# Optimization experiments

Measured on AMD Instinct MI355X. Metric: run time of the kernel, lower is better.

The kernel has to match this reference:

```python
import jax, jax.numpy as jnp
import numpy as np
from jax import lax

EPS = 1e-6
MATCH_THRESHOLD = 0.3
N_DISCRETE_STEPS = 5
DT = 0.01
TWO_PI = 2.0 * np.pi


def setup_inputs() -> dict:
    key = jax.random.key(0)
    ks = jax.random.split(key, 6)
    N, M, D, H, n_osc = 8192, 8192, 4, 64, 28
    detections_t = jax.random.normal(ks[0], (N, D), dtype=jnp.float32)
    detections_t1 = jax.random.normal(ks[1], (M, D), dtype=jnp.float32)
    phase_W1 = jax.random.normal(ks[2], (D, H), dtype=jnp.float32) * (1.0 / np.sqrt(D))
    phase_b1 = jax.random.normal(ks[3], (H,), dtype=jnp.float32) * 0.05
    phase_W2 = jax.random.normal(ks[4], (H, n_osc), dtype=jnp.float32) * (1.0 / np.sqrt(H))
    phase_b2 = jax.random.normal(ks[5], (n_osc,), dtype=jnp.float32) * 0.05
    # fixed oscillator frequencies buffer: [2]*4 + [6]*8 + [40]*16
    frequencies = jnp.concatenate([
        jnp.full((4,), 2.0, jnp.float32),
        jnp.full((8,), 6.0, jnp.float32),
        jnp.full((16,), 40.0, jnp.float32),
    ])
    return {
        'detections_t': detections_t,
        'detections_t1': detections_t1,
        'phase_W1': phase_W1,
        'phase_b1': phase_b1,
        'phase_W2': phase_W2,
        'phase_b2': phase_b2,
        'frequencies': frequencies,
    }


def _encode_phase(x, W1, b1, W2, b2):
    h = jax.nn.relu(x @ W1 + b1)
    raw = h @ W2 + b2
    return raw % TWO_PI  # [N, n_osc]


def _similarity(phase_a, phase_b):
    # real(sum_k e^{i a_k} e^{-i b_k}) = cos(a)@cos(b).T + sin(a)@sin(b).T
    ca, sa = jnp.cos(phase_a), jnp.sin(phase_a)
    cb, sb = jnp.cos(phase_b), jnp.sin(phase_b)
    na = jnp.sqrt(jnp.sum(ca * ca + sa * sa, axis=-1, keepdims=True)) + EPS  # [N,1]
    nb = jnp.sqrt(jnp.sum(cb * cb + sb * sb, axis=-1, keepdims=True)) + EPS  # [M,1]
    sim = (ca @ cb.T + sa @ sb.T) / (na * nb.T)  # [N, M]
    return sim


def reference(detections_t, detections_t1, phase_W1, phase_b1, phase_W2, phase_b2, frequencies):
    phase_t = _encode_phase(detections_t, phase_W1, phase_b1, phase_W2, phase_b2)
    phase_t1 = _encode_phase(detections_t1, phase_W1, phase_b1, phase_W2, phase_b2)

    # uncoupled phase advance (n_discrete_steps fixed small loop)
    phase = phase_t
    for _ in range(N_DISCRETE_STEPS):
        phase = (phase + TWO_PI * frequencies * DT) % TWO_PI

    sim = _similarity(phase, phase_t1)  # [N, M]

    N = detections_t.shape[0]
    M = detections_t1.shape[0]
    max_sims = jnp.max(sim, axis=1)
    max_idxs = jnp.argmax(sim, axis=1)
    order = jnp.argsort(-max_sims)  # descending

    def body(i, carry):
        matches, used = carry
        idx = order[i]
        j = max_idxs[idx]
        ok = jnp.logical_and(jnp.logical_not(used[j]), max_sims[idx] > MATCH_THRESHOLD)
        matches = matches.at[idx].set(jnp.where(ok, j, -1))
        used = used.at[j].set(jnp.logical_or(used[j], ok))
        return (matches, used)

    matches0 = jnp.full((N,), -1, dtype=jnp.int32)
    used0 = jnp.zeros((M,), dtype=bool)
    matches, _ = lax.fori_loop(0, N, body, (matches0, used0))
    return (matches, sim)
```

## Files before the change

kernel.cpp:

```cpp
#include <hip/hip_runtime.h>
#include <math.h>

#define NR 8192
#define N_OSC 28
#define TWO_PI_F 6.28318530717958647692f
#define PLANE 524288

typedef __attribute__((ext_vector_type(8))) short s16x8;
typedef __attribute__((ext_vector_type(16))) float f32x16;
typedef __attribute__((ext_vector_type(4))) float f32x4;
typedef __attribute__((ext_vector_type(4))) unsigned int u32x4;

#define AS3(p) ((__attribute__((address_space(3))) void*)(p))
#define AS1C(p) ((const __attribute__((address_space(1))) void*)(p))

__device__ __forceinline__ float modpos(float x) {
    float r = fmodf(x, TWO_PI_F);
    if (r < 0.0f) r += TWO_PI_F;
    return r;
}
__device__ __forceinline__ unsigned fmono(float f) {
    unsigned u = __float_as_uint(f);
    return (u & 0x80000000u) ? ~u : (u | 0x80000000u);
}
__device__ __forceinline__ unsigned short f2bf(float f) {
    unsigned u = __float_as_uint(f);
    return (unsigned short)((u + 0x7FFFu + ((u >> 16) & 1u)) >> 16);
}
__device__ __forceinline__ float bf2f(unsigned short h) {
    return __uint_as_float(((unsigned)h) << 16);
}


__global__ __launch_bounds__(256, 1) void encode_kernel(
    const float* __restrict__ detA, const float* __restrict__ detB,
    const float* __restrict__ W1, const float* __restrict__ b1,
    const float* __restrict__ W2, const float* __restrict__ b2,
    const float* __restrict__ freq,
    unsigned short* __restrict__ tabA, unsigned short* __restrict__ tabB,
    float* __restrict__ normA, float* __restrict__ normB)
{
    __shared__ float sW1[4 * 64];
    __shared__ float sb1[64];
    __shared__ float sW2[64 * N_OSC];
    __shared__ float sb2[N_OSC];
    __shared__ float sDelta[N_OSC];

    int t = threadIdx.x;
    for (int i = t; i < 4 * 64; i += 256) sW1[i] = W1[i];
    for (int i = t; i < 64; i += 256) sb1[i] = b1[i];
    for (int i = t; i < 64 * N_OSC; i += 256) sW2[i] = W2[i];
    for (int i = t; i < N_OSC; i += 256) {
        sb2[i] = b2[i];
        sDelta[i] = (TWO_PI_F * freq[i]) * 0.01f;
    }
    __syncthreads();

    int gid = blockIdx.x * 256 + t;
    bool isA = gid < NR;
    int row = isA ? gid : gid - NR;
    const float* det = isA ? detA : detB;
    unsigned short* tab = isA ? tabA : tabB;
    float* nrm = isA ? normA : normB;

    float4 xv = *(const float4*)(det + (size_t)row * 4);
    float x0 = xv.x, x1 = xv.y, x2 = xv.z, x3 = xv.w;

    float h[64];
#pragma unroll
    for (int j = 0; j < 64; ++j) {
        float a = x0 * sW1[0 * 64 + j];
        a += x1 * sW1[1 * 64 + j];
        a += x2 * sW1[2 * 64 + j];
        a += x3 * sW1[3 * 64 + j];
        a += sb1[j];
        h[j] = fmaxf(a, 0.0f);
    }

    float raw[N_OSC];
#pragma unroll
    for (int o = 0; o < N_OSC; ++o) raw[o] = 0.0f;
#pragma unroll
    for (int j = 0; j < 64; ++j) {
        float hj = h[j];
#pragma unroll
        for (int o = 0; o < N_OSC; ++o) raw[o] += hj * sW2[j * N_OSC + o];
    }

    unsigned h2[32], m2[32], l2[32];
#pragma unroll
    for (int i = 0; i < 32; ++i) { h2[i] = 0u; m2[i] = 0u; l2[i] = 0u; }

    float csum = 0.0f;
#pragma unroll
    for (int o = 0; o < N_OSC; ++o) {
        float p = raw[o] + sb2[o];
        p = modpos(p);
        if (isA) {
            float d = sDelta[o];
#pragma unroll
            for (int s = 0; s < 5; ++s) { p = modpos(p + d); }
        }
        float sn, cs;
        sincosf(p, &sn, &cs);
        csum += cs * cs + sn * sn;
        {
            unsigned short v0 = f2bf(cs); float r1 = cs - bf2f(v0);
            unsigned short v1 = f2bf(r1); float r2 = r1 - bf2f(v1);
            unsigned short v2 = f2bf(r2);
            const int k = o, i = k >> 1, sh = (k & 1) * 16;
            h2[i] |= ((unsigned)v0) << sh;
            m2[i] |= ((unsigned)v1) << sh;
            l2[i] |= ((unsigned)v2) << sh;
        }
        {
            unsigned short v0 = f2bf(sn); float r1 = sn - bf2f(v0);
            unsigned short v1 = f2bf(r1); float r2 = r1 - bf2f(v1);
            unsigned short v2 = f2bf(r2);
            const int k = 28 + o, i = k >> 1, sh = (k & 1) * 16;
            h2[i] |= ((unsigned)v0) << sh;
            m2[i] |= ((unsigned)v1) << sh;
            l2[i] |= ((unsigned)v2) << sh;
        }
    }

    size_t gbase = (size_t)(row >> 5) * 2048 + (size_t)(row & 31) * 8;
#pragma unroll
    for (int c = 0; c < 8; ++c) {
        size_t off = gbase + (size_t)(c >> 1) * 512 + (size_t)(c & 1) * 256;
        u32x4 vh, vm, vl;
#pragma unroll
        for (int e = 0; e < 4; ++e) {
            vh[e] = h2[c * 4 + e]; vm[e] = m2[c * 4 + e]; vl[e] = l2[c * 4 + e];
        }
        *(u32x4*)(tab + off) = vh;
        *(u32x4*)(tab + PLANE + off) = vm;
        *(u32x4*)(tab + 2 * PLANE + off) = vl;
    }
    nrm[row] = 1.0f / (sqrtf(csum) + 1e-6f);
}

#define MFMA(a, b, c) __builtin_amdgcn_mfma_f32_32x32x16_bf16((a), (b), (c), 0, 0, 0)

__global__ __launch_bounds__(256, 1) void sim_kernel(
    const unsigned short* __restrict__ tabA, const unsigned short* __restrict__ tabB,
    const float* __restrict__ normA, const float* __restrict__ normB,
    float* __restrict__ simOut, unsigned long long* __restrict__ rowMax)
{
    __shared__ __align__(16) unsigned char smem[69632];
    unsigned short* Ash = (unsigned short*)smem;

    int bid = blockIdx.x;
    int swz = (bid & 7) * 512 + (bid >> 3);
    int bx = swz & 63, by = swz >> 6;
    int r0 = by * 128, c0 = bx * 128;

    int t = threadIdx.x, w = t >> 6, l = t & 63;
    int wr = w >> 1, wc = w & 1;
    int lrow = l & 31;
    int gB = (c0 + wc * 64) >> 5;
    int gr0 = r0 >> 5;
    size_t l8 = (size_t)l * 8;

#define GLD(tab, pl, g, ks) \
    (*(const s16x8*)((tab) + (size_t)(pl) * PLANE + (size_t)(g) * 2048 + (size_t)(ks) * 512 + l8))

    s16x8 bh0[4], bh1[4], bm0[4], bm1[4], bl0[4], bl1[4];
#pragma unroll
    for (int ks = 0; ks < 4; ++ks) {
        bh0[ks] = GLD(tabB, 0, gB, ks);  bh1[ks] = GLD(tabB, 0, gB + 1, ks);
        bm0[ks] = GLD(tabB, 1, gB, ks);  bm1[ks] = GLD(tabB, 1, gB + 1, ks);
        bl0[ks] = GLD(tabB, 2, gB, ks);  bl1[ks] = GLD(tabB, 2, gB + 1, ks);
    }
#undef GLD

#pragma unroll
    for (int i = 0; i < 12; ++i) {
        int unit = w * 12 + i;
        int p = unit >> 4, rem = unit & 15;
        int g = rem >> 2, ks = rem & 3;
        const unsigned short* src = tabA + (size_t)p * PLANE
            + (size_t)(gr0 + g) * 2048 + (size_t)ks * 512 + l8;
        __builtin_amdgcn_global_load_lds(AS1C(src), AS3(Ash + unit * 512), 16, 0, 0);
    }
    __builtin_amdgcn_sched_barrier(0);
    __syncthreads();

    f32x16 acc00, acc01, acc10, acc11;
#pragma unroll
    for (int r = 0; r < 16; ++r) { acc00[r] = 0.f; acc01[r] = 0.f; acc10[r] = 0.f; acc11[r] = 0.f; }

    const char* Ab = (const char*)Ash + (size_t)wr * 8192 + (size_t)l * 16;
#define LDA(p, gg, ks) (*(const s16x8*)(Ab + ((p) * 16384 + (gg) * 4096 + (ks) * 1024)))

#pragma unroll
    for (int ks = 0; ks < 4; ++ks) {
        s16x8 ah0 = LDA(0, 0, ks), ah1 = LDA(0, 1, ks);
        s16x8 am0 = LDA(1, 0, ks), am1 = LDA(1, 1, ks);
        s16x8 al0 = LDA(2, 0, ks), al1 = LDA(2, 1, ks);

        acc00 = MFMA(ah0, bh0[ks], acc00); acc01 = MFMA(ah0, bh1[ks], acc01);
        acc10 = MFMA(ah1, bh0[ks], acc10); acc11 = MFMA(ah1, bh1[ks], acc11);
        acc00 = MFMA(ah0, bm0[ks], acc00); acc01 = MFMA(ah0, bm1[ks], acc01);
        acc10 = MFMA(ah1, bm0[ks], acc10); acc11 = MFMA(ah1, bm1[ks], acc11);
        acc00 = MFMA(am0, bh0[ks], acc00); acc01 = MFMA(am0, bh1[ks], acc01);
        acc10 = MFMA(am1, bh0[ks], acc10); acc11 = MFMA(am1, bh1[ks], acc11);
        acc00 = MFMA(am0, bm0[ks], acc00); acc01 = MFMA(am0, bm1[ks], acc01);
        acc10 = MFMA(am1, bm0[ks], acc10); acc11 = MFMA(am1, bm1[ks], acc11);
        acc00 = MFMA(ah0, bl0[ks], acc00); acc01 = MFMA(ah0, bl1[ks], acc01);
        acc10 = MFMA(ah1, bl0[ks], acc10); acc11 = MFMA(ah1, bl1[ks], acc11);
        acc00 = MFMA(al0, bh0[ks], acc00); acc01 = MFMA(al0, bh1[ks], acc01);
        acc10 = MFMA(al1, bh0[ks], acc10); acc11 = MFMA(al1, bh1[ks], acc11);
    }
#undef LDA

    float icn0 = normB[c0 + wc * 64 + lrow];
    float icn1 = normB[c0 + wc * 64 + 32 + lrow];

    __syncthreads();
    float* scr = (float*)(smem + w * 17408);

#pragma unroll
    for (int r = 0; r < 16; ++r) {
        int rd0 = (r & 3) + 8 * (r >> 2) + 4 * (l >> 5);
        float irn0 = normA[r0 + wr * 64 + rd0];
        scr[rd0 * 68 + lrow]      = acc00[r] * (irn0 * icn0);
        scr[rd0 * 68 + 32 + lrow] = acc01[r] * (irn0 * icn1);
        int rd1 = rd0 + 32;
        float irn1 = normA[r0 + wr * 64 + rd1];
        scr[rd1 * 68 + lrow]      = acc10[r] * (irn1 * icn0);
        scr[rd1 * 68 + 32 + lrow] = acc11[r] * (irn1 * icn1);
    }

#pragma unroll
    for (int s = 0; s < 16; ++s) {
        int lr = 4 * s + (l >> 4);
        f32x4 v = *(const f32x4*)&scr[lr * 68 + (l & 15) * 4];
        int grow = r0 + wr * 64 + lr;
        __builtin_nontemporal_store(v,
            (f32x4*)&simOut[(size_t)grow * NR + c0 + wc * 64 + (l & 15) * 4]);
    }

    {
        const float* rp = &scr[l * 68];
        float mv = -2.0f; int mc = 0;
#pragma unroll
        for (int c4 = 0; c4 < 16; ++c4) {
            f32x4 v = *(const f32x4*)&rp[c4 * 4];
#pragma unroll
            for (int e = 0; e < 4; ++e) {
                bool g = v[e] > mv;
                mv = g ? v[e] : mv;
                mc = g ? c4 * 4 + e : mc;
            }
        }
        int grow = r0 + wr * 64 + l;
        unsigned gcol = (unsigned)(c0 + wc * 64 + mc);
        unsigned long long key = ((unsigned long long)fmono(mv) << 32)
                               | (unsigned long long)(0xFFFFFFFFu - gcol);
        atomicMax(&rowMax[grow], key);
    }
}

__global__ __launch_bounds__(256) void rowwin_kernel(
    const unsigned long long* __restrict__ rowMax,
    unsigned long long* __restrict__ colWin,
    float* __restrict__ outMatches)
{
    int r = blockIdx.x * 256 + threadIdx.x;
    if (r >= NR) return;
    outMatches[r] = -1.0f;
    unsigned long long key = rowMax[r];
    unsigned m = (unsigned)(key >> 32);
    unsigned bits = (m & 0x80000000u) ? (m ^ 0x80000000u) : ~m;
    float ms = __uint_as_float(bits);
    unsigned col = 0xFFFFFFFFu - (unsigned)key;
    if (ms > 0.3f) {
        unsigned long long ck = ((unsigned long long)m << 32)
                              | (unsigned long long)(0xFFFFFFFFu - (unsigned)r);
        atomicMax(&colWin[col], ck);
    }
}

__global__ __launch_bounds__(256) void colfin_kernel(
    const unsigned long long* __restrict__ colWin,
    float* __restrict__ outMatches)
{
    int j = blockIdx.x * 256 + threadIdx.x;
    if (j >= NR) return;
    unsigned long long w = colWin[j];
    if (w != 0ull) {
        unsigned r = 0xFFFFFFFFu - (unsigned)w;
        outMatches[r] = (float)j;
    }
}

extern "C" void kernel_launch(void* const* d_in, const int* in_sizes, int n_in,
                              void* d_out, int out_size, void* d_ws, size_t ws_size,
                              hipStream_t stream) {
    const float* detA = (const float*)d_in[0];
    const float* detB = (const float*)d_in[1];
    const float* W1   = (const float*)d_in[2];
    const float* b1   = (const float*)d_in[3];
    const float* W2   = (const float*)d_in[4];
    const float* b2   = (const float*)d_in[5];
    const float* freq = (const float*)d_in[6];
    float* out = (float*)d_out;

    char* ws = (char*)d_ws;
    unsigned short* tabA = (unsigned short*)(ws);
    unsigned short* tabB = (unsigned short*)(ws + 3145728);
    float* normA = (float*)(ws + 6291456);
    float* normB = (float*)(ws + 6324224);
    unsigned long long* rowMax = (unsigned long long*)(ws + 6356992);
    unsigned long long* colWin = (unsigned long long*)(ws + 6422528);

    (void)hipMemsetAsync(rowMax, 0, NR * 8, stream);
    (void)hipMemsetAsync(colWin, 0, NR * 8, stream);

    encode_kernel<<<64, 256, 0, stream>>>(detA, detB, W1, b1, W2, b2, freq,
                                          tabA, tabB, normA, normB);
    sim_kernel<<<4096, 256, 0, stream>>>(tabA, tabB, normA, normB, out + NR, rowMax);
    rowwin_kernel<<<NR / 256, 256, 0, stream>>>(rowMax, colWin, out);
    colfin_kernel<<<NR / 256, 256, 0, stream>>>(colWin, out);
}
```

Before: 149.4 us.

## Fold norms into encoded phases, shrink sim tiles, compute row max from registers

Normalization is folded into the encode step by scaling cos and sin by the inverse norm before bf16 splitting, which drops the norm loads and multiplies from the similarity epilogue. The sim kernel moves to 64x128 tiles with 2 waves per block and twice as many blocks, and swaps the MFMA operand order so each lane's accumulators hold a row. The row argmax is then computed directly from accumulator registers plus a cross-half shuffle, instead of rescanning shared memory. The cost is a transposed shared-memory write pattern with stride 65 and more blocks each reloading the B tiles, plus slightly different rounding because normalization now happens before the bf16 split.

```diff
diff --git a/kernel.cpp b/kernel.cpp
--- a/kernel.cpp
+++ b/kernel.cpp
@@ -37,8 +37,7 @@
     const float* __restrict__ W1, const float* __restrict__ b1,
     const float* __restrict__ W2, const float* __restrict__ b2,
     const float* __restrict__ freq,
-    unsigned short* __restrict__ tabA, unsigned short* __restrict__ tabB,
-    float* __restrict__ normA, float* __restrict__ normB)
+    unsigned short* __restrict__ tabA, unsigned short* __restrict__ tabB)
 {
     __shared__ float sW1[4 * 64];
     __shared__ float sb1[64];
@@ -61,7 +60,6 @@
     int row = isA ? gid : gid - NR;
     const float* det = isA ? detA : detB;
     unsigned short* tab = isA ? tabA : tabB;
-    float* nrm = isA ? normA : normB;
 
     float4 xv = *(const float4*)(det + (size_t)row * 4);
     float x0 = xv.x, x1 = xv.y, x2 = xv.z, x3 = xv.w;
@@ -87,10 +85,7 @@
         for (int o = 0; o < N_OSC; ++o) raw[o] += hj * sW2[j * N_OSC + o];
     }
 
-    unsigned h2[32], m2[32], l2[32];
-#pragma unroll
-    for (int i = 0; i < 32; ++i) { h2[i] = 0u; m2[i] = 0u; l2[i] = 0u; }
-
+    float cv[N_OSC], sv[N_OSC];
     float csum = 0.0f;
 #pragma unroll
     for (int o = 0; o < N_OSC; ++o) {
@@ -103,9 +98,20 @@
         }
         float sn, cs;
         sincosf(p, &sn, &cs);
+        cv[o] = cs; sv[o] = sn;
         csum += cs * cs + sn * sn;
+    }
+    float irn = 1.0f / (sqrtf(csum) + 1e-6f);
+
+    unsigned h2[32], m2[32], l2[32];
+#pragma unroll
+    for (int i = 0; i < 32; ++i) { h2[i] = 0u; m2[i] = 0u; l2[i] = 0u; }
+
+#pragma unroll
+    for (int o = 0; o < N_OSC; ++o) {
         {
-            unsigned short v0 = f2bf(cs); float r1 = cs - bf2f(v0);
+            float x = cv[o] * irn;
+            unsigned short v0 = f2bf(x); float r1 = x - bf2f(v0);
             unsigned short v1 = f2bf(r1); float r2 = r1 - bf2f(v1);
             unsigned short v2 = f2bf(r2);
             const int k = o, i = k >> 1, sh = (k & 1) * 16;
@@ -114,7 +120,8 @@
             l2[i] |= ((unsigned)v2) << sh;
         }
         {
-            unsigned short v0 = f2bf(sn); float r1 = sn - bf2f(v0);
+            float x = sv[o] * irn;
+            unsigned short v0 = f2bf(x); float r1 = x - bf2f(v0);
             unsigned short v1 = f2bf(r1); float r2 = r1 - bf2f(v1);
             unsigned short v2 = f2bf(r2);
             const int k = 28 + o, i = k >> 1, sh = (k & 1) * 16;
@@ -137,27 +144,25 @@
         *(u32x4*)(tab + PLANE + off) = vm;
         *(u32x4*)(tab + 2 * PLANE + off) = vl;
     }
-    nrm[row] = 1.0f / (sqrtf(csum) + 1e-6f);
 }
 
 #define MFMA(a, b, c) __builtin_amdgcn_mfma_f32_32x32x16_bf16((a), (b), (c), 0, 0, 0)
 
-__global__ __launch_bounds__(256, 1) void sim_kernel(
+__global__ __launch_bounds__(128, 1) void sim_kernel(
     const unsigned short* __restrict__ tabA, const unsigned short* __restrict__ tabB,
-    const float* __restrict__ normA, const float* __restrict__ normB,
     float* __restrict__ simOut, unsigned long long* __restrict__ rowMax)
 {
-    __shared__ __align__(16) unsigned char smem[69632];
+    __shared__ __align__(16) unsigned char smem[33280];
     unsigned short* Ash = (unsigned short*)smem;
 
     int bid = blockIdx.x;
-    int swz = (bid & 7) * 512 + (bid >> 3);
+    int swz = (bid & 7) * 1024 + (bid >> 3);
     int bx = swz & 63, by = swz >> 6;
-    int r0 = by * 128, c0 = bx * 128;
+    int r0 = by * 64, c0 = bx * 128;
 
     int t = threadIdx.x, w = t >> 6, l = t & 63;
-    int wr = w >> 1, wc = w & 1;
-    int lrow = l & 31;
+    int wc = w;
+    int l31 = l & 31, h5 = l >> 5;
     int gB = (c0 + wc * 64) >> 5;
     int gr0 = r0 >> 5;
     size_t l8 = (size_t)l * 8;
@@ -177,7 +182,7 @@
 #pragma unroll
     for (int i = 0; i < 12; ++i) {
         int unit = w * 12 + i;
-        int p = unit >> 4, rem = unit & 15;
+        int p = unit >> 3, rem = unit & 7;
         int g = rem >> 2, ks = rem & 3;
         const unsigned short* src = tabA + (size_t)p * PLANE
             + (size_t)(gr0 + g) * 2048 + (size_t)ks * 512 + l8;
@@ -190,8 +195,8 @@
 #pragma unroll
     for (int r = 0; r < 16; ++r) { acc00[r] = 0.f; acc01[r] = 0.f; acc10[r] = 0.f; acc11[r] = 0.f; }
 
-    const char* Ab = (const char*)Ash + (size_t)wr * 8192 + (size_t)l * 16;
-#define LDA(p, gg, ks) (*(const s16x8*)(Ab + ((p) * 16384 + (gg) * 4096 + (ks) * 1024)))
+    const char* Ab = (const char*)Ash + (size_t)l * 16;
+#define LDA(p, g, ks) (*(const s16x8*)(Ab + (((p) * 8 + (g) * 4 + (ks)) * 1024)))
 
 #pragma unroll
     for (int ks = 0; ks < 4; ++ks) {
@@ -199,66 +204,71 @@
         s16x8 am0 = LDA(1, 0, ks), am1 = LDA(1, 1, ks);
         s16x8 al0 = LDA(2, 0, ks), al1 = LDA(2, 1, ks);
 
-        acc00 = MFMA(ah0, bh0[ks], acc00); acc01 = MFMA(ah0, bh1[ks], acc01);
-        acc10 = MFMA(ah1, bh0[ks], acc10); acc11 = MFMA(ah1, bh1[ks], acc11);
-        acc00 = MFMA(ah0, bm0[ks], acc00); acc01 = MFMA(ah0, bm1[ks], acc01);
-        acc10 = MFMA(ah1, bm0[ks], acc10); acc11 = MFMA(ah1, bm1[ks], acc11);
-        acc00 = MFMA(am0, bh0[ks], acc00); acc01 = MFMA(am0, bh1[ks], acc01);
-        acc10 = MFMA(am1, bh0[ks], acc10); acc11 = MFMA(am1, bh1[ks], acc11);
-        acc00 = MFMA(am0, bm0[ks], acc00); acc01 = MFMA(am0, bm1[ks], acc01);
-        acc10 = MFMA(am1, bm0[ks], acc10); acc11 = MFMA(am1, bm1[ks], acc11);
-        acc00 = MFMA(ah0, bl0[ks], acc00); acc01 = MFMA(ah0, bl1[ks], acc01);
-        acc10 = MFMA(ah1, bl0[ks], acc10); acc11 = MFMA(ah1, bl1[ks], acc11);
-        acc00 = MFMA(al0, bh0[ks], acc00); acc01 = MFMA(al0, bh1[ks], acc01);
-        acc10 = MFMA(al1, bh0[ks], acc10); acc11 = MFMA(al1, bh1[ks], acc11);
+        acc00 = MFMA(bh0[ks], ah0, acc00); acc01 = MFMA(bh1[ks], ah0, acc01);
+        acc10 = MFMA(bh0[ks], ah1, acc10); acc11 = MFMA(bh1[ks], ah1, acc11);
+        acc00 = MFMA(bm0[ks], ah0, acc00); acc01 = MFMA(bm1[ks], ah0, acc01);
+        acc10 = MFMA(bm0[ks], ah1, acc10); acc11 = MFMA(bm1[ks], ah1, acc11);
+        acc00 = MFMA(bh0[ks], am0, acc00); acc01 = MFMA(bh1[ks], am0, acc01);
+        acc10 = MFMA(bh0[ks], am1, acc10); acc11 = MFMA(bh1[ks], am1, acc11);
+        acc00 = MFMA(bm0[ks], am0, acc00); acc01 = MFMA(bm1[ks], am0, acc01);
+        acc10 = MFMA(bm0[ks], am1, acc10); acc11 = MFMA(bm1[ks], am1, acc11);
+        acc00 = MFMA(bl0[ks], ah0, acc00); acc01 = MFMA(bl1[ks], ah0, acc01);
+        acc10 = MFMA(bl0[ks], ah1, acc10); acc11 = MFMA(bl1[ks], ah1, acc11);
+        acc00 = MFMA(bh0[ks], al0, acc00); acc01 = MFMA(bh1[ks], al0, acc01);
+        acc10 = MFMA(bh0[ks], al1, acc10); acc11 = MFMA(bh1[ks], al1, acc11);
     }
 #undef LDA
 
-    float icn0 = normB[c0 + wc * 64 + lrow];
-    float icn1 = normB[c0 + wc * 64 + 32 + lrow];
+    int cbase = c0 + wc * 64 + 4 * h5;
+    unsigned long long key0 = 0ull, key1 = 0ull;
+#pragma unroll
+    for (int r = 0; r < 16; ++r) {
+        int pa = (r & 3) + 8 * (r >> 2);
+        unsigned col0 = (unsigned)(cbase + pa);
+        unsigned col1 = (unsigned)(cbase + 32 + pa);
+        unsigned long long k;
+        k = ((unsigned long long)fmono(acc00[r]) << 32) | (unsigned long long)(0xFFFFFFFFu - col0);
+        if (k > key0) key0 = k;
+        k = ((unsigned long long)fmono(acc01[r]) << 32) | (unsigned long long)(0xFFFFFFFFu - col1);
+        if (k > key0) key0 = k;
+        k = ((unsigned long long)fmono(acc10[r]) << 32) | (unsigned long long)(0xFFFFFFFFu - col0);
+        if (k > key1) key1 = k;
+        k = ((unsigned long long)fmono(acc11[r]) << 32) | (unsigned long long)(0xFFFFFFFFu - col1);
+        if (k > key1) key1 = k;
+    }
+    {
+        unsigned lo = (unsigned)key0, hi = (unsigned)(key0 >> 32);
+        unsigned olo = __shfl_xor(lo, 32, 64), ohi = __shfl_xor(hi, 32, 64);
+        unsigned long long o = ((unsigned long long)ohi << 32) | olo;
+        if (o > key0) key0 = o;
+        lo = (unsigned)key1; hi = (unsigned)(key1 >> 32);
+        olo = __shfl_xor(lo, 32, 64); ohi = __shfl_xor(hi, 32, 64);
+        o = ((unsigned long long)ohi << 32) | olo;
+        if (o > key1) key1 = o;
+    }
+    if (l < 32) {
+        atomicMax(&rowMax[r0 + l], key0);
+        atomicMax(&rowMax[r0 + 32 + l], key1);
+    }
 
     __syncthreads();
-    float* scr = (float*)(smem + w * 17408);
+    float* scr = (float*)(smem + w * 16640);
 
 #pragma unroll
     for (int r = 0; r < 16; ++r) {
-        int rd0 = (r & 3) + 8 * (r >> 2) + 4 * (l >> 5);
-        float irn0 = normA[r0 + wr * 64 + rd0];
-        scr[rd0 * 68 + lrow]      = acc00[r] * (irn0 * icn0);
-        scr[rd0 * 68 + 32 + lrow] = acc01[r] * (irn0 * icn1);
-        int rd1 = rd0 + 32;
-        float irn1 = normA[r0 + wr * 64 + rd1];
-        scr[rd1 * 68 + lrow]      = acc10[r] * (irn1 * icn0);
-        scr[rd1 * 68 + 32 + lrow] = acc11[r] * (irn1 * icn1);
+        int pa = (r & 3) + 8 * (r >> 2) + 4 * h5;
+        scr[l31 * 65 + pa]             = acc00[r];
+        scr[l31 * 65 + 32 + pa]        = acc01[r];
+        scr[(32 + l31) * 65 + pa]      = acc10[r];
+        scr[(32 + l31) * 65 + 32 + pa] = acc11[r];
     }
 
 #pragma unroll
     for (int s = 0; s < 16; ++s) {
         int lr = 4 * s + (l >> 4);
-        f32x4 v = *(const f32x4*)&scr[lr * 68 + (l & 15) * 4];
-        int grow = r0 + wr * 64 + lr;
+        f32x4 v = *(const f32x4*)&scr[lr * 65 + (l & 15) * 4];
         __builtin_nontemporal_store(v,
-            (f32x4*)&simOut[(size_t)grow * NR + c0 + wc * 64 + (l & 15) * 4]);
-    }
-
-    {
-        const float* rp = &scr[l * 68];
-        float mv = -2.0f; int mc = 0;
-#pragma unroll
-        for (int c4 = 0; c4 < 16; ++c4) {
-            f32x4 v = *(const f32x4*)&rp[c4 * 4];
-#pragma unroll
-            for (int e = 0; e < 4; ++e) {
-                bool g = v[e] > mv;
-                mv = g ? v[e] : mv;
-                mc = g ? c4 * 4 + e : mc;
-            }
-        }
-        int grow = r0 + wr * 64 + l;
-        unsigned gcol = (unsigned)(c0 + wc * 64 + mc);
-        unsigned long long key = ((unsigned long long)fmono(mv) << 32)
-                               | (unsigned long long)(0xFFFFFFFFu - gcol);
-        atomicMax(&rowMax[grow], key);
+            (f32x4*)&simOut[(size_t)(r0 + lr) * NR + c0 + wc * 64 + (l & 15) * 4]);
     }
 }
 
@@ -310,17 +320,15 @@
     char* ws = (char*)d_ws;
     unsigned short* tabA = (unsigned short*)(ws);
     unsigned short* tabB = (unsigned short*)(ws + 3145728);
-    float* normA = (float*)(ws + 6291456);
-    float* normB = (float*)(ws + 6324224);
-    unsigned long long* rowMax = (unsigned long long*)(ws + 6356992);
-    unsigned long long* colWin = (unsigned long long*)(ws + 6422528);
+    unsigned long long* rowMax = (unsigned long long*)(ws + 6291456);
+    unsigned long long* colWin = (unsigned long long*)(ws + 6356992);
 
     (void)hipMemsetAsync(rowMax, 0, NR * 8, stream);
     (void)hipMemsetAsync(colWin, 0, NR * 8, stream);
 
     encode_kernel<<<64, 256, 0, stream>>>(detA, detB, W1, b1, W2, b2, freq,
-                                          tabA, tabB, normA, normB);
-    sim_kernel<<<4096, 256, 0, stream>>>(tabA, tabB, normA, normB, out + NR, rowMax);
+                                          tabA, tabB);
+    sim_kernel<<<8192, 128, 0, stream>>>(tabA, tabB, out + NR, rowMax);
     rowwin_kernel<<<NR / 256, 256, 0, stream>>>(rowMax, colWin, out);
     colfin_kernel<<<NR / 256, 256, 0, stream>>>(colWin, out);
 }
```

Result: faster. 142.1 us (-4.9%).

## Stage B tile in LDS and stream A planes with double-buffered loads

Applied to the files above, without the earlier changes.

Moves the three B bf16 planes into shared memory instead of registers and streams A planes one at a time through two LDS buffers, overlapping the next plane's load with MFMA work on the current one. It relaxes launch bounds to permit higher occupancy and zeroes the rowMax/colWin buffers inside the encode kernel instead of separate memset calls. This trades register pressure for more LDS reads and extra barriers per tile.

```diff
diff --git a/kernel.cpp b/kernel.cpp
--- a/kernel.cpp
+++ b/kernel.cpp
@@ -32,13 +32,14 @@
 }
 
 
-__global__ __launch_bounds__(256, 1) void encode_kernel(
+__global__ __launch_bounds__(256) void encode_kernel(
     const float* __restrict__ detA, const float* __restrict__ detB,
     const float* __restrict__ W1, const float* __restrict__ b1,
     const float* __restrict__ W2, const float* __restrict__ b2,
     const float* __restrict__ freq,
     unsigned short* __restrict__ tabA, unsigned short* __restrict__ tabB,
-    float* __restrict__ normA, float* __restrict__ normB)
+    float* __restrict__ normA, float* __restrict__ normB,
+    unsigned long long* __restrict__ rowMax, unsigned long long* __restrict__ colWin)
 {
     __shared__ float sW1[4 * 64];
     __shared__ float sb1[64];
@@ -62,6 +63,8 @@
     const float* det = isA ? detA : detB;
     unsigned short* tab = isA ? tabA : tabB;
     float* nrm = isA ? normA : normB;
+
+    if (isA) rowMax[gid] = 0ull; else colWin[gid - NR] = 0ull;
 
     float4 xv = *(const float4*)(det + (size_t)row * 4);
     float x0 = xv.x, x1 = xv.y, x2 = xv.z, x3 = xv.w;
@@ -140,15 +143,12 @@
     nrm[row] = 1.0f / (sqrtf(csum) + 1e-6f);
 }
 
-#define MFMA(a, b, c) __builtin_amdgcn_mfma_f32_32x32x16_bf16((a), (b), (c), 0, 0, 0)
-
-__global__ __launch_bounds__(256, 1) void sim_kernel(
+__global__ __launch_bounds__(256) void sim_kernel(
     const unsigned short* __restrict__ tabA, const unsigned short* __restrict__ tabB,
     const float* __restrict__ normA, const float* __restrict__ normB,
     float* __restrict__ simOut, unsigned long long* __restrict__ rowMax)
 {
-    __shared__ __align__(16) unsigned char smem[69632];
-    unsigned short* Ash = (unsigned short*)smem;
+    __shared__ __align__(16) unsigned char smem[81920];
 
     int bid = blockIdx.x;
     int swz = (bid & 7) * 512 + (bid >> 3);
@@ -158,61 +158,99 @@
     int t = threadIdx.x, w = t >> 6, l = t & 63;
     int wr = w >> 1, wc = w & 1;
     int lrow = l & 31;
-    int gB = (c0 + wc * 64) >> 5;
-    int gr0 = r0 >> 5;
+    int gA0 = r0 >> 5, gB0 = c0 >> 5;
     size_t l8 = (size_t)l * 8;
-
-#define GLD(tab, pl, g, ks) \
-    (*(const s16x8*)((tab) + (size_t)(pl) * PLANE + (size_t)(g) * 2048 + (size_t)(ks) * 512 + l8))
-
-    s16x8 bh0[4], bh1[4], bm0[4], bm1[4], bl0[4], bl1[4];
-#pragma unroll
-    for (int ks = 0; ks < 4; ++ks) {
-        bh0[ks] = GLD(tabB, 0, gB, ks);  bh1[ks] = GLD(tabB, 0, gB + 1, ks);
-        bm0[ks] = GLD(tabB, 1, gB, ks);  bm1[ks] = GLD(tabB, 1, gB + 1, ks);
-        bl0[ks] = GLD(tabB, 2, gB, ks);  bl1[ks] = GLD(tabB, 2, gB + 1, ks);
-    }
-#undef GLD
 
 #pragma unroll
     for (int i = 0; i < 12; ++i) {
         int unit = w * 12 + i;
         int p = unit >> 4, rem = unit & 15;
         int g = rem >> 2, ks = rem & 3;
-        const unsigned short* src = tabA + (size_t)p * PLANE
-            + (size_t)(gr0 + g) * 2048 + (size_t)ks * 512 + l8;
-        __builtin_amdgcn_global_load_lds(AS1C(src), AS3(Ash + unit * 512), 16, 0, 0);
-    }
-    __builtin_amdgcn_sched_barrier(0);
-    __syncthreads();
+        const unsigned short* src = tabB + (size_t)p * PLANE
+            + (size_t)(gB0 + g) * 2048 + (size_t)ks * 512 + l8;
+        __builtin_amdgcn_global_load_lds(AS1C(src), AS3(smem + unit * 1024), 16, 0, 0);
+    }
+#pragma unroll
+    for (int i = 0; i < 4; ++i) {
+        int unit = w * 4 + i;
+        int g = unit >> 2, ks = unit & 3;
+        const unsigned short* src = tabA
+            + (size_t)(gA0 + g) * 2048 + (size_t)ks * 512 + l8;
+        __builtin_amdgcn_global_load_lds(AS1C(src), AS3(smem + 49152 + unit * 1024), 16, 0, 0);
+    }
+    __syncthreads();
+#pragma unroll
+    for (int i = 0; i < 4; ++i) {
+        int unit = w * 4 + i;
+        int g = unit >> 2, ks = unit & 3;
+        const unsigned short* src = tabA + PLANE
+            + (size_t)(gA0 + g) * 2048 + (size_t)ks * 512 + l8;
+        __builtin_amdgcn_global_load_lds(AS1C(src), AS3(smem + 65536 + unit * 1024), 16, 0, 0);
+    }
 
     f32x16 acc00, acc01, acc10, acc11;
 #pragma unroll
     for (int r = 0; r < 16; ++r) { acc00[r] = 0.f; acc01[r] = 0.f; acc10[r] = 0.f; acc11[r] = 0.f; }
 
-    const char* Ab = (const char*)Ash + (size_t)wr * 8192 + (size_t)l * 16;
-#define LDA(p, gg, ks) (*(const s16x8*)(Ab + ((p) * 16384 + (gg) * 4096 + (ks) * 1024)))
+#define LDB(p, gg, ks) (*(const s16x8*)(smem + (((p) * 16 + (2 * wc + (gg)) * 4 + (ks)) * 1024) + (size_t)l * 16))
+#define LDA(buf, gg, ks) (*(const s16x8*)(smem + 49152 + (buf) * 16384 + (((2 * wr + (gg)) * 4 + (ks)) * 1024) + (size_t)l * 16))
+
+    s16x8 bh0[4], bh1[4];
 
 #pragma unroll
     for (int ks = 0; ks < 4; ++ks) {
-        s16x8 ah0 = LDA(0, 0, ks), ah1 = LDA(0, 1, ks);
-        s16x8 am0 = LDA(1, 0, ks), am1 = LDA(1, 1, ks);
-        s16x8 al0 = LDA(2, 0, ks), al1 = LDA(2, 1, ks);
-
-        acc00 = MFMA(ah0, bh0[ks], acc00); acc01 = MFMA(ah0, bh1[ks], acc01);
-        acc10 = MFMA(ah1, bh0[ks], acc10); acc11 = MFMA(ah1, bh1[ks], acc11);
-        acc00 = MFMA(ah0, bm0[ks], acc00); acc01 = MFMA(ah0, bm1[ks], acc01);
-        acc10 = MFMA(ah1, bm0[ks], acc10); acc11 = MFMA(ah1, bm1[ks], acc11);
-        acc00 = MFMA(am0, bh0[ks], acc00); acc01 = MFMA(am0, bh1[ks], acc01);
-        acc10 = MFMA(am1, bh0[ks], acc10); acc11 = MFMA(am1, bh1[ks], acc11);
-        acc00 = MFMA(am0, bm0[ks], acc00); acc01 = MFMA(am0, bm1[ks], acc01);
-        acc10 = MFMA(am1, bm0[ks], acc10); acc11 = MFMA(am1, bm1[ks], acc11);
-        acc00 = MFMA(ah0, bl0[ks], acc00); acc01 = MFMA(ah0, bl1[ks], acc01);
-        acc10 = MFMA(ah1, bl0[ks], acc10); acc11 = MFMA(ah1, bl1[ks], acc11);
-        acc00 = MFMA(al0, bh0[ks], acc00); acc01 = MFMA(al0, bh1[ks], acc01);
-        acc10 = MFMA(al1, bh0[ks], acc10); acc11 = MFMA(al1, bh1[ks], acc11);
+        s16x8 a0 = LDA(0, 0, ks), a1 = LDA(0, 1, ks);
+        bh0[ks] = LDB(0, 0, ks); bh1[ks] = LDB(0, 1, ks);
+        acc00 = __builtin_amdgcn_mfma_f32_32x32x16_bf16(a0, bh0[ks], acc00, 0, 0, 0);
+        acc01 = __builtin_amdgcn_mfma_f32_32x32x16_bf16(a0, bh1[ks], acc01, 0, 0, 0);
+        acc10 = __builtin_amdgcn_mfma_f32_32x32x16_bf16(a1, bh0[ks], acc10, 0, 0, 0);
+        acc11 = __builtin_amdgcn_mfma_f32_32x32x16_bf16(a1, bh1[ks], acc11, 0, 0, 0);
+        s16x8 b0 = LDB(1, 0, ks), b1 = LDB(1, 1, ks);
+        acc00 = __builtin_amdgcn_mfma_f32_32x32x16_bf16(a0, b0, acc00, 0, 0, 0);
+        acc01 = __builtin_amdgcn_mfma_f32_32x32x16_bf16(a0, b1, acc01, 0, 0, 0);
+        acc10 = __builtin_amdgcn_mfma_f32_32x32x16_bf16(a1, b0, acc10, 0, 0, 0);
+        acc11 = __builtin_amdgcn_mfma_f32_32x32x16_bf16(a1, b1, acc11, 0, 0, 0);
+        b0 = LDB(2, 0, ks); b1 = LDB(2, 1, ks);
+        acc00 = __builtin_amdgcn_mfma_f32_32x32x16_bf16(a0, b0, acc00, 0, 0, 0);
+        acc01 = __builtin_amdgcn_mfma_f32_32x32x16_bf16(a0, b1, acc01, 0, 0, 0);
+        acc10 = __builtin_amdgcn_mfma_f32_32x32x16_bf16(a1, b0, acc10, 0, 0, 0);
+        acc11 = __builtin_amdgcn_mfma_f32_32x32x16_bf16(a1, b1, acc11, 0, 0, 0);
+    }
+    __syncthreads();
+#pragma unroll
+    for (int i = 0; i < 4; ++i) {
+        int unit = w * 4 + i;
+        int g = unit >> 2, ks = unit & 3;
+        const unsigned short* src = tabA + 2 * PLANE
+            + (size_t)(gA0 + g) * 2048 + (size_t)ks * 512 + l8;
+        __builtin_amdgcn_global_load_lds(AS1C(src), AS3(smem + 49152 + unit * 1024), 16, 0, 0);
+    }
+
+#pragma unroll
+    for (int ks = 0; ks < 4; ++ks) {
+        s16x8 a0 = LDA(1, 0, ks), a1 = LDA(1, 1, ks);
+        acc00 = __builtin_amdgcn_mfma_f32_32x32x16_bf16(a0, bh0[ks], acc00, 0, 0, 0);
+        acc01 = __builtin_amdgcn_mfma_f32_32x32x16_bf16(a0, bh1[ks], acc01, 0, 0, 0);
+        acc10 = __builtin_amdgcn_mfma_f32_32x32x16_bf16(a1, bh0[ks], acc10, 0, 0, 0);
+        acc11 = __builtin_amdgcn_mfma_f32_32x32x16_bf16(a1, bh1[ks], acc11, 0, 0, 0);
+        s16x8 b0 = LDB(1, 0, ks), b1 = LDB(1, 1, ks);
+        acc00 = __builtin_amdgcn_mfma_f32_32x32x16_bf16(a0, b0, acc00, 0, 0, 0);
+        acc01 = __builtin_amdgcn_mfma_f32_32x32x16_bf16(a0, b1, acc01, 0, 0, 0);
+        acc10 = __builtin_amdgcn_mfma_f32_32x32x16_bf16(a1, b0, acc10, 0, 0, 0);
+        acc11 = __builtin_amdgcn_mfma_f32_32x32x16_bf16(a1, b1, acc11, 0, 0, 0);
+    }
+    __syncthreads();
+
+#pragma unroll
+    for (int ks = 0; ks < 4; ++ks) {
+        s16x8 a0 = LDA(0, 0, ks), a1 = LDA(0, 1, ks);
+        acc00 = __builtin_amdgcn_mfma_f32_32x32x16_bf16(a0, bh0[ks], acc00, 0, 0, 0);
+        acc01 = __builtin_amdgcn_mfma_f32_32x32x16_bf16(a0, bh1[ks], acc01, 0, 0, 0);
+        acc10 = __builtin_amdgcn_mfma_f32_32x32x16_bf16(a1, bh0[ks], acc10, 0, 0, 0);
+        acc11 = __builtin_amdgcn_mfma_f32_32x32x16_bf16(a1, bh1[ks], acc11, 0, 0, 0);
     }
 #undef LDA
+#undef LDB
 
     float icn0 = normB[c0 + wc * 64 + lrow];
     float icn1 = normB[c0 + wc * 64 + 32 + lrow];
@@ -315,11 +353,8 @@
     unsigned long long* rowMax = (unsigned long long*)(ws + 6356992);
     unsigned long long* colWin = (unsigned long long*)(ws + 6422528);
 
-    (void)hipMemsetAsync(rowMax, 0, NR * 8, stream);
-    (void)hipMemsetAsync(colWin, 0, NR * 8, stream);
-
     encode_kernel<<<64, 256, 0, stream>>>(detA, detB, W1, b1, W2, b2, freq,
-                                          tabA, tabB, normA, normB);
+                                          tabA, tabB, normA, normB, rowMax, colWin);
     sim_kernel<<<4096, 256, 0, stream>>>(tabA, tabB, normA, normB, out + NR, rowMax);
     rowwin_kernel<<<NR / 256, 256, 0, stream>>>(rowMax, colWin, out);
     colfin_kernel<<<NR / 256, 256, 0, stream>>>(colWin, out);
```

Measured after the change: 134.1 us. -10.3%, faster.
